# Performance work log

Measured on AMD Instinct MI355X. Metric: run time of the kernel, lower is better.

The kernel has to match this reference:

```python
import jax, jax.numpy as jnp
import numpy as np

N, D, B, O, E = 4096, 1024, 512, 1, 16  # samples, in_size, bottleneck, out_size, n_tasks
L1_LAMBDA = 1e-4


def setup_inputs() -> dict:
    key = jax.random.key(0)
    ks = jax.random.split(key, 6)
    x = jax.random.normal(ks[0], (N, D), jnp.float32)
    keys = jax.random.randint(ks[1], (N,), 0, E, dtype=jnp.int32)
    W1 = jax.random.normal(ks[2], (E, B, D), jnp.float32) / np.sqrt(D).astype(np.float32)
    b1 = jax.random.normal(ks[3], (E, B), jnp.float32) * 0.01
    W2 = jax.random.normal(ks[4], (E, O, B), jnp.float32) / np.sqrt(B).astype(np.float32)
    b2 = jax.random.normal(ks[5], (E, O), jnp.float32) * 0.01
    return {"x": x, "keys": keys, "W1": W1, "b1": b1, "W2": W2, "b2": b2}


def reference(x, keys, W1, b1, W2, b2):
    """Per-sample task-specific 2-layer bottleneck MLP dispatch.

    x: [N, D] float; keys: [N] int task indices.
    W1: [E, B, D], b1: [E, B], W2: [E, O, B], b2: [E, O].
    Returns (out [N, O], l1_lambda * sum_n L1(params of expert keys[n])).
    """
    n = x.shape[0]
    e = W1.shape[0]
    # Dense MoE dispatch: first linear for all experts, then select per sample.
    h_all = jnp.einsum('nd,ebd->neb', x, W1) + b1[None]          # [N, E, B]
    h = h_all[jnp.arange(n), keys]                                # [N, B]
    h = jax.nn.relu(h)                                            # activation='relu'
    out = jnp.einsum('nb,nob->no', h, W2[keys]) + b2[keys]        # [N, O]
    # L1 of the selected expert's parameters is accumulated once per sample.
    l1_per_expert = (jnp.abs(W1).sum((1, 2)) + jnp.abs(b1).sum(1)
                     + jnp.abs(W2).sum((1, 2)) + jnp.abs(b2).sum(1))  # [E]
    counts = jnp.zeros((e,), x.dtype).at[keys].add(jnp.ones((), x.dtype))
    l1 = jnp.asarray(L1_LAMBDA, x.dtype) * jnp.dot(counts, l1_per_expert)
    return out, l1
```

## Files before the change

kernel.cpp:

```cpp
#include <hip/hip_runtime.h>
#include <hip/hip_bf16.h>

#define N_S 4096
#define D_IN 1024
#define B_BOT 512
#define E_EXP 16
#define L1_LAMBDA 1e-4f

#define MT 64
#define NT 128
#define KC 64
#define MT_GRID 6
#define IDSTR 512

typedef float f32x4 __attribute__((ext_vector_type(4)));
typedef short bf16x8 __attribute__((ext_vector_type(8)));
typedef unsigned int u32;


__device__ __forceinline__ ushort4 cvt4(float4 v) {
    union { __hip_bfloat162 b2[2]; ushort4 u4; } u;
    u.b2[0] = __float22bfloat162_rn({v.x, v.y});
    u.b2[1] = __float22bfloat162_rn({v.z, v.w});
    return u.u4;
}

__device__ __forceinline__ void async16(const ushort* g, ushort* l) {
    __builtin_amdgcn_global_load_lds(
        (const __attribute__((address_space(1))) u32*)g,
        (__attribute__((address_space(3))) u32*)l, 16, 0, 0);
}

__global__ __launch_bounds__(256)
void prep_kernel(const float* __restrict__ x, const int* __restrict__ keys,
                 const float* __restrict__ W1, const float* __restrict__ b1,
                 const float* __restrict__ W2, const float* __restrict__ b2,
                 float* __restrict__ out, int* __restrict__ counts,
                 float* __restrict__ l1small, float* __restrict__ l1part,
                 int* __restrict__ ids, ushort* __restrict__ W1b,
                 ushort* __restrict__ xb) {
    const int blk = blockIdx.x;
    const int t = threadIdx.x;
    if (blk < E_EXP) {
        const int e = blk;
        out[e * 256 + t] = 0.f;
        float s = fabsf(b1[e * B_BOT + t]) + fabsf(b1[e * B_BOT + 256 + t])
                + fabsf(W2[e * B_BOT + t]) + fabsf(W2[e * B_BOT + 256 + t]);
        if (t == 0) s += fabsf(b2[e]);
#pragma unroll
        for (int off = 32; off > 0; off >>= 1) s += __shfl_down(s, off);
        __shared__ float ws4a[4];
        __shared__ int cnt_s;
        if ((t & 63) == 0) ws4a[t >> 6] = s;
        if (t == 0) cnt_s = 0;
        __syncthreads();
        if (t == 0) l1small[e] = ws4a[0] + ws4a[1] + ws4a[2] + ws4a[3];
        const int lane = t & 63;
        for (int it = 0; it < N_S / 256; ++it) {
            const int i = it * 256 + t;
            const bool m = (keys[i] == e);
            const unsigned long long mask = __ballot(m);
            int base = 0;
            if (lane == 0) base = atomicAdd(&cnt_s, __popcll(mask));
            base = __shfl(base, 0);
            if (m) {
                const int pos = base + __popcll(mask & ((1ull << lane) - 1ull));
                if (pos < IDSTR) ids[e * IDSTR + pos] = i;
            }
        }
        __syncthreads();
        if (t == 0) counts[e] = min(cnt_s, IDSTR);
    } else if (blk < E_EXP + 1024) {
        const int i = blk - E_EXP;
        const long long base = (long long)i * 2048;
        const float4* __restrict__ src = (const float4*)W1;
        ushort4* __restrict__ dst = (ushort4*)W1b;
        float s = 0.f;
#pragma unroll
        for (int m = 0; m < 8; ++m) {
            const long long idx = base + m * 256 + t;
            float4 v = src[idx];
            s += fabsf(v.x) + fabsf(v.y) + fabsf(v.z) + fabsf(v.w);
            dst[idx] = cvt4(v);
        }
#pragma unroll
        for (int off = 32; off > 0; off >>= 1) s += __shfl_down(s, off);
        __shared__ float ws4b[4];
        if ((t & 63) == 0) ws4b[t >> 6] = s;
        __syncthreads();
        if (t == 0) l1part[i] = ws4b[0] + ws4b[1] + ws4b[2] + ws4b[3];
    } else {
        const int i = blk - E_EXP - 1024;
        const long long base = (long long)i * 2048;
        const float4* __restrict__ src = (const float4*)x;
        ushort4* __restrict__ dst = (ushort4*)xb;
#pragma unroll
        for (int m = 0; m < 8; ++m) {
            const long long idx = base + m * 256 + t;
            dst[idx] = cvt4(src[idx]);
        }
    }
}

__global__ __launch_bounds__(256, 2)
void mlp_kernel(const ushort* __restrict__ W1b, const ushort* __restrict__ xb,
                const float* __restrict__ b1, const float* __restrict__ W2,
                const float* __restrict__ b2, const int* __restrict__ counts,
                const float* __restrict__ l1small, const float* __restrict__ l1part,
                const int* __restrict__ ids, float* __restrict__ out) {
    const int mt = blockIdx.x, nb = blockIdx.y, e = blockIdx.z;
    const int t = threadIdx.x, wave = t >> 6, lane = t & 63;
    const int l15 = lane & 15, qd = lane >> 4;
    const int wm = wave & 1, wn = wave >> 1;

    __shared__ __align__(16) ushort As[MT * KC];
    __shared__ __align__(16) ushort Bs[NT * KC];
    __shared__ int sid_s[MT];
    __shared__ float red[4][32];

    if (mt == 0 && nb == 0 && e == 0 && wave == 0) {
        const int el = lane >> 2, sub = lane & 3;
        float s = 0.f;
#pragma unroll
        for (int k = 0; k < 16; ++k) s += l1part[el * 64 + sub * 16 + k];
        s += __shfl_xor(s, 1);
        s += __shfl_xor(s, 2);
        float v = (sub == 0) ? (float)counts[el] * (s + l1small[el]) : 0.f;
        v += __shfl_xor(v, 4);
        v += __shfl_xor(v, 8);
        v += __shfl_xor(v, 16);
        v += __shfl_xor(v, 32);
        if (lane == 0) out[N_S] = L1_LAMBDA * v;
    }

    const int cnt = counts[e];
    const int m0 = mt * MT;
    if (m0 >= cnt) return;

    if (t < MT) sid_s[t] = ids[e * IDSTR + min(m0 + t, cnt - 1)];
    __syncthreads();

    const int colb = nb * NT;
    float b1v[4], w2v[4];
#pragma unroll
    for (int j = 0; j < 4; ++j) {
        const int col = colb + 64 * wn + 16 * j + l15;
        b1v[j] = b1[e * B_BOT + col];
        w2v[j] = W2[e * B_BOT + col];
    }
    const float b2e = b2[e];

    const ushort* gA[2];
    ushort* dA[2];
#pragma unroll
    for (int p = 0; p < 2; ++p) {
        const int u = p * 256 + t, r = u >> 3;
        const int q = (u & 7) ^ (r & 7);
        gA[p] = xb + (size_t)sid_s[r] * D_IN + q * 8;
        dA[p] = As + (size_t)(p * 256 + wave * 64) * 8;
    }
    const ushort* gB[4];
    ushort* dB[4];
#pragma unroll
    for (int p = 0; p < 4; ++p) {
        const int u = p * 256 + t, r = u >> 3;
        const int q = (u & 7) ^ (r & 7);
        gB[p] = W1b + (size_t)(e * B_BOT + colb + r) * D_IN + q * 8;
        dB[p] = Bs + (size_t)(p * 256 + wave * 64) * 8;
    }

    const ushort* fA[2][2];
#pragma unroll
    for (int i = 0; i < 2; ++i)
#pragma unroll
        for (int s = 0; s < 2; ++s) {
            const int r = 32 * wm + 16 * i + l15;
            fA[i][s] = As + (size_t)(r * 8 + ((s * 4 + qd) ^ (r & 7))) * 8;
        }
    const ushort* fB[4][2];
#pragma unroll
    for (int j = 0; j < 4; ++j)
#pragma unroll
        for (int s = 0; s < 2; ++s) {
            const int r = 64 * wn + 16 * j + l15;
            fB[j][s] = Bs + (size_t)(r * 8 + ((s * 4 + qd) ^ (r & 7))) * 8;
        }

    f32x4 acc[2][4];
#pragma unroll
    for (int i = 0; i < 2; ++i)
#pragma unroll
        for (int j = 0; j < 4; ++j) acc[i][j] = (f32x4){0.f, 0.f, 0.f, 0.f};

    for (int c = 0; c < D_IN / KC; ++c) {
        const int ko = c * KC;
        __syncthreads();
#pragma unroll
        for (int p = 0; p < 2; ++p) async16(gA[p] + ko, dA[p]);
#pragma unroll
        for (int p = 0; p < 4; ++p) async16(gB[p] + ko, dB[p]);
        __syncthreads();
#pragma unroll
        for (int s = 0; s < 2; ++s) {
            bf16x8 a0 = *(const bf16x8*)fA[0][s];
            bf16x8 a1 = *(const bf16x8*)fA[1][s];
            bf16x8 bb[4];
#pragma unroll
            for (int j = 0; j < 4; ++j) bb[j] = *(const bf16x8*)fB[j][s];
#pragma unroll
            for (int j = 0; j < 4; ++j) {
                acc[0][j] = __builtin_amdgcn_mfma_f32_16x16x32_bf16(a0, bb[j], acc[0][j], 0, 0, 0);
                acc[1][j] = __builtin_amdgcn_mfma_f32_16x16x32_bf16(a1, bb[j], acc[1][j], 0, 0, 0);
            }
        }
    }

    float p[2][4] = {{0.f, 0.f, 0.f, 0.f}, {0.f, 0.f, 0.f, 0.f}};
#pragma unroll
    for (int j = 0; j < 4; ++j)
#pragma unroll
        for (int i = 0; i < 2; ++i)
#pragma unroll
            for (int r = 0; r < 4; ++r) {
                const float h = fmaxf(acc[i][j][r] + b1v[j], 0.f);
                p[i][r] = fmaf(h, w2v[j], p[i][r]);
            }
#pragma unroll
    for (int off = 8; off > 0; off >>= 1)
#pragma unroll
        for (int i = 0; i < 2; ++i)
#pragma unroll
            for (int r = 0; r < 4; ++r) p[i][r] += __shfl_xor(p[i][r], off, 16);

    if (l15 == 0) {
#pragma unroll
        for (int i = 0; i < 2; ++i)
#pragma unroll
            for (int r = 0; r < 4; ++r)
                red[wn][32 * wm + 16 * i + 4 * qd + r] = p[i][r];
    }
    __syncthreads();
    if (t < MT) {
        const int m = m0 + t;
        if (m < cnt) {
            float v = red[0][t] + red[1][t];
            if (nb == 0) v += b2e;
            atomicAdd(&out[ids[e * IDSTR + m]], v);
        }
    }
}

extern "C" void kernel_launch(void* const* d_in, const int* in_sizes, int n_in,
                              void* d_out, int out_size, void* d_ws, size_t ws_size,
                              hipStream_t stream) {
    const float* x    = (const float*)d_in[0];
    const int*   keys = (const int*)d_in[1];
    const float* W1   = (const float*)d_in[2];
    const float* b1   = (const float*)d_in[3];
    const float* W2   = (const float*)d_in[4];
    const float* b2   = (const float*)d_in[5];
    float* out = (float*)d_out;

    char* ws = (char*)d_ws;
    int*    counts  = (int*)(ws + 0);
    float*  l1small = (float*)(ws + 64);
    float*  l1part  = (float*)(ws + 128);
    int*    ids     = (int*)(ws + 4224);
    ushort* W1b     = (ushort*)(ws + 65536);
    ushort* xb      = (ushort*)(ws + 65536 + 16777216);

    prep_kernel<<<E_EXP + 1024 + 512, 256, 0, stream>>>(
        x, keys, W1, b1, W2, b2, out, counts, l1small, l1part, ids, W1b, xb);
    mlp_kernel<<<dim3(MT_GRID, 4, E_EXP), 256, 0, stream>>>(
        W1b, xb, b1, W2, b2, counts, l1small, l1part, ids, out);
}
```

Baseline: 116.3 us.

## Double-buffer register-staged LDS loads and use persistent 256-block grid

Replaces the async global-to-LDS loads and single LDS buffer with register-staged double buffering, so the next K-chunk's global loads overlap the MFMA work on the current chunk and one barrier per iteration is removed. The grid becomes a flat 256 blocks with experts and column tiles interleaved, and each block loops over row tiles with a stride of four tiles instead of one block per tile. The aim is to hide memory latency and balance the uneven per-expert counts. In exchange LDS use doubles, register pressure rises from the staged values, and a block now processes several row tiles one after another.

Measured after the change: 126.6 us. 1.09x slower.

```diff
diff --git a/kernel.cpp b/kernel.cpp
--- a/kernel.cpp
+++ b/kernel.cpp
@@ -10,12 +10,10 @@
 #define MT 64
 #define NT 128
 #define KC 64
-#define MT_GRID 6
 #define IDSTR 512
 
 typedef float f32x4 __attribute__((ext_vector_type(4)));
 typedef short bf16x8 __attribute__((ext_vector_type(8)));
-typedef unsigned int u32;
 
 
 __device__ __forceinline__ ushort4 cvt4(float4 v) {
@@ -23,12 +21,6 @@
     u.b2[0] = __float22bfloat162_rn({v.x, v.y});
     u.b2[1] = __float22bfloat162_rn({v.z, v.w});
     return u.u4;
-}
-
-__device__ __forceinline__ void async16(const ushort* g, ushort* l) {
-    __builtin_amdgcn_global_load_lds(
-        (const __attribute__((address_space(1))) u32*)g,
-        (__attribute__((address_space(3))) u32*)l, 16, 0, 0);
 }
 
 __global__ __launch_bounds__(256)
@@ -108,17 +100,18 @@
                 const float* __restrict__ b2, const int* __restrict__ counts,
                 const float* __restrict__ l1small, const float* __restrict__ l1part,
                 const int* __restrict__ ids, float* __restrict__ out) {
-    const int mt = blockIdx.x, nb = blockIdx.y, e = blockIdx.z;
+    const int b = blockIdx.x;
+    const int mt = b >> 6, e = (b & 63) >> 2, nb = b & 3;
     const int t = threadIdx.x, wave = t >> 6, lane = t & 63;
     const int l15 = lane & 15, qd = lane >> 4;
     const int wm = wave & 1, wn = wave >> 1;
 
-    __shared__ __align__(16) ushort As[MT * KC];
-    __shared__ __align__(16) ushort Bs[NT * KC];
+    __shared__ __align__(16) ushort As[2 * MT * KC];
+    __shared__ __align__(16) ushort Bs[2 * NT * KC];
     __shared__ int sid_s[MT];
-    __shared__ float red[4][32];
-
-    if (mt == 0 && nb == 0 && e == 0 && wave == 0) {
+    __shared__ float red[2][MT];
+
+    if (b == 0 && wave == 0) {
         const int el = lane >> 2, sub = lane & 3;
         float s = 0.f;
 #pragma unroll
@@ -134,11 +127,7 @@
     }
 
     const int cnt = counts[e];
-    const int m0 = mt * MT;
-    if (m0 >= cnt) return;
-
-    if (t < MT) sid_s[t] = ids[e * IDSTR + min(m0 + t, cnt - 1)];
-    __syncthreads();
+    if (mt * MT >= cnt) return;
 
     const int colb = nb * NT;
     float b1v[4], w2v[4];
@@ -150,103 +139,142 @@
     }
     const float b2e = b2[e];
 
-    const ushort* gA[2];
-    ushort* dA[2];
-#pragma unroll
-    for (int p = 0; p < 2; ++p) {
-        const int u = p * 256 + t, r = u >> 3;
-        const int q = (u & 7) ^ (r & 7);
-        gA[p] = xb + (size_t)sid_s[r] * D_IN + q * 8;
-        dA[p] = As + (size_t)(p * 256 + wave * 64) * 8;
-    }
     const ushort* gB[4];
-    ushort* dB[4];
 #pragma unroll
     for (int p = 0; p < 4; ++p) {
         const int u = p * 256 + t, r = u >> 3;
-        const int q = (u & 7) ^ (r & 7);
-        gB[p] = W1b + (size_t)(e * B_BOT + colb + r) * D_IN + q * 8;
-        dB[p] = Bs + (size_t)(p * 256 + wave * 64) * 8;
-    }
-
-    const ushort* fA[2][2];
+        const int g = (u & 7) ^ (r & 7);
+        gB[p] = W1b + (size_t)(e * B_BOT + colb + r) * D_IN + g * 8;
+    }
+    const int dst = t * 8;
+
+    int offA[2][2], offB[4][2];
 #pragma unroll
     for (int i = 0; i < 2; ++i)
 #pragma unroll
         for (int s = 0; s < 2; ++s) {
             const int r = 32 * wm + 16 * i + l15;
-            fA[i][s] = As + (size_t)(r * 8 + ((s * 4 + qd) ^ (r & 7))) * 8;
-        }
-    const ushort* fB[4][2];
+            offA[i][s] = (r * 8 + ((s * 4 + qd) ^ (r & 7))) * 8;
+        }
 #pragma unroll
     for (int j = 0; j < 4; ++j)
 #pragma unroll
         for (int s = 0; s < 2; ++s) {
             const int r = 64 * wn + 16 * j + l15;
-            fB[j][s] = Bs + (size_t)(r * 8 + ((s * 4 + qd) ^ (r & 7))) * 8;
-        }
-
-    f32x4 acc[2][4];
-#pragma unroll
-    for (int i = 0; i < 2; ++i)
-#pragma unroll
-        for (int j = 0; j < 4; ++j) acc[i][j] = (f32x4){0.f, 0.f, 0.f, 0.f};
-
-    for (int c = 0; c < D_IN / KC; ++c) {
-        const int ko = c * KC;
-        __syncthreads();
-#pragma unroll
-        for (int p = 0; p < 2; ++p) async16(gA[p] + ko, dA[p]);
-#pragma unroll
-        for (int p = 0; p < 4; ++p) async16(gB[p] + ko, dB[p]);
-        __syncthreads();
-#pragma unroll
-        for (int s = 0; s < 2; ++s) {
-            bf16x8 a0 = *(const bf16x8*)fA[0][s];
-            bf16x8 a1 = *(const bf16x8*)fA[1][s];
-            bf16x8 bb[4];
-#pragma unroll
-            for (int j = 0; j < 4; ++j) bb[j] = *(const bf16x8*)fB[j][s];
-#pragma unroll
-            for (int j = 0; j < 4; ++j) {
-                acc[0][j] = __builtin_amdgcn_mfma_f32_16x16x32_bf16(a0, bb[j], acc[0][j], 0, 0, 0);
-                acc[1][j] = __builtin_amdgcn_mfma_f32_16x16x32_bf16(a1, bb[j], acc[1][j], 0, 0, 0);
-            }
-        }
-    }
-
-    float p[2][4] = {{0.f, 0.f, 0.f, 0.f}, {0.f, 0.f, 0.f, 0.f}};
-#pragma unroll
-    for (int j = 0; j < 4; ++j)
+            offB[j][s] = (r * 8 + ((s * 4 + qd) ^ (r & 7))) * 8;
+        }
+
+    for (int m0 = mt * MT; m0 < cnt; m0 += 4 * MT) {
+        if (t < MT) sid_s[t] = ids[e * IDSTR + min(m0 + t, cnt - 1)];
+        __syncthreads();
+
+        const ushort* gA[2];
+#pragma unroll
+        for (int p = 0; p < 2; ++p) {
+            const int u = p * 256 + t, r = u >> 3;
+            const int g = (u & 7) ^ (r & 7);
+            gA[p] = xb + (size_t)sid_s[r] * D_IN + g * 8;
+        }
+
+        f32x4 acc[2][4];
 #pragma unroll
         for (int i = 0; i < 2; ++i)
 #pragma unroll
-            for (int r = 0; r < 4; ++r) {
-                const float h = fmaxf(acc[i][j][r] + b1v[j], 0.f);
-                p[i][r] = fmaf(h, w2v[j], p[i][r]);
-            }
-#pragma unroll
-    for (int off = 8; off > 0; off >>= 1)
-#pragma unroll
-        for (int i = 0; i < 2; ++i)
-#pragma unroll
-            for (int r = 0; r < 4; ++r) p[i][r] += __shfl_xor(p[i][r], off, 16);
-
-    if (l15 == 0) {
-#pragma unroll
-        for (int i = 0; i < 2; ++i)
-#pragma unroll
-            for (int r = 0; r < 4; ++r)
-                red[wn][32 * wm + 16 * i + 4 * qd + r] = p[i][r];
-    }
-    __syncthreads();
-    if (t < MT) {
-        const int m = m0 + t;
-        if (m < cnt) {
-            float v = red[0][t] + red[1][t];
-            if (nb == 0) v += b2e;
-            atomicAdd(&out[ids[e * IDSTR + m]], v);
-        }
+            for (int j = 0; j < 4; ++j) acc[i][j] = (f32x4){0.f, 0.f, 0.f, 0.f};
+
+        {
+            uint4 ra0 = *(const uint4*)(gA[0]);
+            uint4 ra1 = *(const uint4*)(gA[1]);
+            uint4 rb0 = *(const uint4*)(gB[0]);
+            uint4 rb1 = *(const uint4*)(gB[1]);
+            uint4 rb2 = *(const uint4*)(gB[2]);
+            uint4 rb3 = *(const uint4*)(gB[3]);
+            *(uint4*)(As + dst)        = ra0;
+            *(uint4*)(As + 2048 + dst) = ra1;
+            *(uint4*)(Bs + dst)        = rb0;
+            *(uint4*)(Bs + 2048 + dst) = rb1;
+            *(uint4*)(Bs + 4096 + dst) = rb2;
+            *(uint4*)(Bs + 6144 + dst) = rb3;
+        }
+        __syncthreads();
+
+        for (int c = 0; c < D_IN / KC; ++c) {
+            const int buf = c & 1;
+            const ushort* Ab = As + buf * (MT * KC);
+            const ushort* Bb = Bs + buf * (NT * KC);
+            const bool more = (c + 1 < D_IN / KC);
+            uint4 ra[2], rb[4];
+            if (more) {
+                const int ko = (c + 1) * KC;
+#pragma unroll
+                for (int p = 0; p < 2; ++p) ra[p] = *(const uint4*)(gA[p] + ko);
+#pragma unroll
+                for (int p = 0; p < 4; ++p) rb[p] = *(const uint4*)(gB[p] + ko);
+            }
+#pragma unroll
+            for (int s = 0; s < 2; ++s) {
+                bf16x8 a0 = *(const bf16x8*)(Ab + offA[0][s]);
+                bf16x8 a1 = *(const bf16x8*)(Ab + offA[1][s]);
+                bf16x8 bb0 = *(const bf16x8*)(Bb + offB[0][s]);
+                bf16x8 bb1 = *(const bf16x8*)(Bb + offB[1][s]);
+                bf16x8 bb2 = *(const bf16x8*)(Bb + offB[2][s]);
+                bf16x8 bb3 = *(const bf16x8*)(Bb + offB[3][s]);
+                acc[0][0] = __builtin_amdgcn_mfma_f32_16x16x32_bf16(a0, bb0, acc[0][0], 0, 0, 0);
+                acc[0][1] = __builtin_amdgcn_mfma_f32_16x16x32_bf16(a0, bb1, acc[0][1], 0, 0, 0);
+                acc[0][2] = __builtin_amdgcn_mfma_f32_16x16x32_bf16(a0, bb2, acc[0][2], 0, 0, 0);
+                acc[0][3] = __builtin_amdgcn_mfma_f32_16x16x32_bf16(a0, bb3, acc[0][3], 0, 0, 0);
+                acc[1][0] = __builtin_amdgcn_mfma_f32_16x16x32_bf16(a1, bb0, acc[1][0], 0, 0, 0);
+                acc[1][1] = __builtin_amdgcn_mfma_f32_16x16x32_bf16(a1, bb1, acc[1][1], 0, 0, 0);
+                acc[1][2] = __builtin_amdgcn_mfma_f32_16x16x32_bf16(a1, bb2, acc[1][2], 0, 0, 0);
+                acc[1][3] = __builtin_amdgcn_mfma_f32_16x16x32_bf16(a1, bb3, acc[1][3], 0, 0, 0);
+            }
+            if (more) {
+                ushort* An = As + (buf ^ 1) * (MT * KC);
+                ushort* Bn = Bs + (buf ^ 1) * (NT * KC);
+                *(uint4*)(An + dst)        = ra[0];
+                *(uint4*)(An + 2048 + dst) = ra[1];
+                *(uint4*)(Bn + dst)        = rb[0];
+                *(uint4*)(Bn + 2048 + dst) = rb[1];
+                *(uint4*)(Bn + 4096 + dst) = rb[2];
+                *(uint4*)(Bn + 6144 + dst) = rb[3];
+            }
+            __syncthreads();
+        }
+
+        float p[2][4] = {{0.f, 0.f, 0.f, 0.f}, {0.f, 0.f, 0.f, 0.f}};
+#pragma unroll
+        for (int j = 0; j < 4; ++j)
+#pragma unroll
+            for (int i = 0; i < 2; ++i)
+#pragma unroll
+                for (int r = 0; r < 4; ++r) {
+                    const float h = fmaxf(acc[i][j][r] + b1v[j], 0.f);
+                    p[i][r] = fmaf(h, w2v[j], p[i][r]);
+                }
+#pragma unroll
+        for (int off = 8; off > 0; off >>= 1)
+#pragma unroll
+            for (int i = 0; i < 2; ++i)
+#pragma unroll
+                for (int r = 0; r < 4; ++r) p[i][r] += __shfl_xor(p[i][r], off, 16);
+
+        if (l15 == 0) {
+#pragma unroll
+            for (int i = 0; i < 2; ++i)
+#pragma unroll
+                for (int r = 0; r < 4; ++r)
+                    red[wn][32 * wm + 16 * i + 4 * qd + r] = p[i][r];
+        }
+        __syncthreads();
+        if (t < MT) {
+            const int m = m0 + t;
+            if (m < cnt) {
+                float v = red[0][t] + red[1][t];
+                if (nb == 0) v += b2e;
+                atomicAdd(&out[ids[e * IDSTR + m]], v);
+            }
+        }
+        __syncthreads();
     }
 }
 
@@ -271,6 +299,6 @@
 
     prep_kernel<<<E_EXP + 1024 + 512, 256, 0, stream>>>(
         x, keys, W1, b1, W2, b2, out, counts, l1small, l1part, ids, W1b, xb);
-    mlp_kernel<<<dim3(MT_GRID, 4, E_EXP), 256, 0, stream>>>(
+    mlp_kernel<<<256, 256, 0, stream>>>(
         W1b, xb, b1, W2, b2, counts, l1small, l1part, ids, out);
 }
```
